# Optimization experiments

Measured on AMD Instinct MI355X. Metric: run time of the kernel, lower is better.

Reference implementation:

```python
import jax, jax.numpy as jnp
import numpy as np

NEG_INF = -10000.0
START_TAG = -2  # index into tag axis
END_TAG = -1


def setup_inputs() -> dict:
    B, T, N = 512, 1024, 64
    key = jax.random.key(0)
    k_h, k_tr, k_len = jax.random.split(key, 3)
    h = jax.random.normal(k_h, (B, T, N), dtype=jnp.float32)
    trans = jax.random.normal(k_tr, (N, N), dtype=jnp.float32)
    lengths = jax.random.randint(k_len, (B,), 1, T + 1)
    lengths = lengths.at[0].set(T)  # ensure max(lengths) == T, as the torch loop assumes
    return {"h": h, "trans": trans, "lengths": lengths}


def reference(h, trans, lengths):
    # h: [B, T, N] emissions; trans: [N, N], trans[i, j] = score(j -> i); lengths: [B]
    B, T, N = h.shape
    mask = jnp.arange(T)[None, :] < lengths[:, None]  # [B, T]

    init = jnp.full((B, N), NEG_INF, dtype=h.dtype).at[:, START_TAG].set(0.0)

    def step(score, xs):
        emit_t, m_t = xs  # emit_t: [B, N], m_t: [B]
        # score_t[b, i] = logsumexp_j( score[b, j] + emit_t[b, i] + trans[i, j] )
        s = score[:, None, :] + emit_t[:, :, None] + trans[None, :, :]  # [B, N, N]
        s = jax.nn.logsumexp(s, axis=2)  # [B, N]
        score = jnp.where(m_t[:, None], s, score)
        return score, None

    score, _ = jax.lax.scan(step, init, (jnp.swapaxes(h, 0, 1), mask.T))
    # terminal transition to END tag, then log-partition
    return jax.nn.logsumexp(score + trans[END_TAG], axis=-1)  # [B]
```

## Files before the change

kernel.cpp:

```cpp
#include <hip/hip_runtime.h>

#define LOG2E 1.4426950408889634f
#define LN2   0.6931471805599453f

__device__ __forceinline__ float bcast(float v, int l) {
  return __uint_as_float(__builtin_amdgcn_readlane(__float_as_uint(v), l));
}

template <bool FWD>
__device__ __forceinline__ void run_chain(
    const float* __restrict__ hb, const float* __restrict__ trans,
    int lane, int len, int nsteps, int T, float& pOut, int& b2Out) {
  constexpr int N = 64;

  float Mreg[N];
  if (FWD) {
    const float4* trow = (const float4*)(trans + lane * N);
#pragma unroll
    for (int q = 0; q < 16; ++q) {
      float4 tq = trow[q];
      Mreg[4 * q + 0] = __builtin_amdgcn_exp2f(tq.x * LOG2E);
      Mreg[4 * q + 1] = __builtin_amdgcn_exp2f(tq.y * LOG2E);
      Mreg[4 * q + 2] = __builtin_amdgcn_exp2f(tq.z * LOG2E);
      Mreg[4 * q + 3] = __builtin_amdgcn_exp2f(tq.w * LOG2E);
    }
  } else {
#pragma unroll
    for (int i = 0; i < N; ++i)
      Mreg[i] = __builtin_amdgcn_exp2f(trans[i * N + lane] * LOG2E);
  }
#pragma unroll
  for (int q = 0; q < 8; ++q) {
    asm volatile("" : "+v"(Mreg[8 * q + 0]), "+v"(Mreg[8 * q + 1]),
                      "+v"(Mreg[8 * q + 2]), "+v"(Mreg[8 * q + 3]),
                      "+v"(Mreg[8 * q + 4]), "+v"(Mreg[8 * q + 5]),
                      "+v"(Mreg[8 * q + 6]), "+v"(Mreg[8 * q + 7]));
  }

  float p;
  if (FWD)
    p = __builtin_amdgcn_exp2f((hb[lane] + trans[lane * N + (N - 2)]) * LOG2E);
  else
    p = __builtin_amdgcn_exp2f(trans[(N - 1) * N + lane] * LOG2E);
  int base2 = 0;

  auto step = [&](float D) {
    float src = FWD ? p : p * D;
    float a0 = 0.f, a1 = 0.f, a2 = 0.f, a3 = 0.f;
#pragma unroll
    for (int j = 0; j < N; j += 4) {
      a0 = fmaf(Mreg[j + 0], bcast(src, j + 0), a0);
      a1 = fmaf(Mreg[j + 1], bcast(src, j + 1), a1);
      a2 = fmaf(Mreg[j + 2], bcast(src, j + 2), a2);
      a3 = fmaf(Mreg[j + 3], bcast(src, j + 3), a3);
    }
    float s = (a0 + a1) + (a2 + a3);
    p = FWD ? s * D : s;
  };

  auto rescale = [&]() {
    unsigned bits = __builtin_amdgcn_readfirstlane(__float_as_uint(p));
    int e = (int)((bits >> 23) & 0xffu);
    base2 += e - 127;
    p *= __uint_as_float((unsigned)(254 - e) << 23);
  };

  auto emit_of = [&](int s) -> float {
    int sc = s < nsteps ? s : nsteps;
    if (sc < 1) sc = 1;
    int t = FWD ? sc : len - sc;
    return __builtin_amdgcn_exp2f(hb[(size_t)t * N + lane] * LOG2E);
  };

  float eb[8];
#pragma unroll
  for (int u = 0; u < 8; ++u) eb[u] = emit_of(1 + u);

  int s = 1;
  for (; s + 8 <= nsteps + 1; s += 8) {
#pragma unroll
    for (int u = 0; u < 8; ++u) {
      step(eb[u]);
      if (u == 3 || u == 7) rescale();
      eb[u] = emit_of(s + u + 8);
    }
  }
  for (; s <= nsteps; ++s) {
    step(eb[(s - 1) & 7]);
    rescale();
  }

  pOut = p;
  b2Out = base2;
}

__global__ __launch_bounds__(128)
__attribute__((amdgpu_waves_per_eu(1, 1)))
void crf_fwd_33852932227637(
    const float* __restrict__ h,
    const float* __restrict__ trans,
    const int* __restrict__ lengths,
    float* __restrict__ out,
    int T) {
  constexpr int N = 64;
  const int b = blockIdx.x;
  const int lane = threadIdx.x & 63;
  const int wv = threadIdx.x >> 6;

  const float* hb = h + (size_t)b * T * N;
  const int len = lengths[b];
  const int m = (len - 1) >> 1;

  float p;
  int b2;
  if (wv == 0)
    run_chain<true>(hb, trans, lane, len, m, T, p, b2);
  else
    run_chain<false>(hb, trans, lane, len, len - 1 - m, T, p, b2);

  __shared__ float xbeta[N];
  __shared__ int xb2;
  if (wv == 1) {
    xbeta[lane] = p;
    if (lane == 0) xb2 = b2;
  }
  __syncthreads();
  if (wv == 0) {
    float z = p * xbeta[lane];
#pragma unroll
    for (int off = 32; off >= 1; off >>= 1)
      z += __shfl_xor(z, off, 64);
    if (lane == 0)
      out[b] = LN2 * ((float)(b2 + xb2) + __builtin_amdgcn_logf(z));
  }
}

extern "C" void kernel_launch(void* const* d_in, const int* in_sizes, int n_in,
                              void* d_out, int out_size, void* d_ws, size_t ws_size,
                              hipStream_t stream) {
  const float* h = (const float*)d_in[0];
  const float* trans = (const float*)d_in[1];
  const int* lengths = (const int*)d_in[2];
  float* out = (float*)d_out;
  const int B = in_sizes[2];
  const int N = 64;
  const int T = in_sizes[0] / (B * N);
  crf_fwd_33852932227637<<<B, N * 2, 0, stream>>>(h, trans, lengths, out, T);
}
```

Before: 281.6 us.

## Broadcast CRF state via LDS float4 reads instead of readlane

```diff
diff --git a/kernel.cpp b/kernel.cpp
--- a/kernel.cpp
+++ b/kernel.cpp
@@ -3,14 +3,10 @@
 #define LOG2E 1.4426950408889634f
 #define LN2   0.6931471805599453f
 
-__device__ __forceinline__ float bcast(float v, int l) {
-  return __uint_as_float(__builtin_amdgcn_readlane(__float_as_uint(v), l));
-}
-
 template <bool FWD>
 __device__ __forceinline__ void run_chain(
     const float* __restrict__ hb, const float* __restrict__ trans,
-    int lane, int len, int nsteps, int T, float& pOut, int& b2Out) {
+    float* __restrict__ pbuf, int lane, int len, int nsteps, int& b2Out) {
   constexpr int N = 64;
 
   float Mreg[N];
@@ -37,38 +33,52 @@
                       "+v"(Mreg[8 * q + 6]), "+v"(Mreg[8 * q + 7]));
   }
 
-  float p;
-  if (FWD)
-    p = __builtin_amdgcn_exp2f((hb[lane] + trans[lane * N + (N - 2)]) * LOG2E);
-  else
-    p = __builtin_amdgcn_exp2f(trans[(N - 1) * N + lane] * LOG2E);
+  {
+    float v;
+    if (FWD) {
+      v = __builtin_amdgcn_exp2f((hb[lane] + trans[lane * N + (N - 2)]) * LOG2E);
+    } else {
+      v = __builtin_amdgcn_exp2f(trans[(N - 1) * N + lane] * LOG2E);
+      if (nsteps >= 1)
+        v *= __builtin_amdgcn_exp2f(hb[(size_t)(len - 1) * N + lane] * LOG2E);
+    }
+    pbuf[lane] = v;
+  }
   int base2 = 0;
 
-  auto step = [&](float D) {
-    float src = FWD ? p : p * D;
-    float a0 = 0.f, a1 = 0.f, a2 = 0.f, a3 = 0.f;
+  const int ns = FWD ? nsteps : nsteps - 1;
+
+  auto step = [&](float D, bool resc) {
+    const float4* pb4 = (const float4*)pbuf;
+    float a[8] = {0.f, 0.f, 0.f, 0.f, 0.f, 0.f, 0.f, 0.f};
+    float p0ref = 0.f;
 #pragma unroll
-    for (int j = 0; j < N; j += 4) {
-      a0 = fmaf(Mreg[j + 0], bcast(src, j + 0), a0);
-      a1 = fmaf(Mreg[j + 1], bcast(src, j + 1), a1);
-      a2 = fmaf(Mreg[j + 2], bcast(src, j + 2), a2);
-      a3 = fmaf(Mreg[j + 3], bcast(src, j + 3), a3);
+    for (int g = 0; g < 16; ++g) {
+      float4 q = pb4[g];
+      if (g == 0) p0ref = q.x;
+      const int b0 = (4 * g) & 7;
+      a[b0 + 0] = fmaf(Mreg[4 * g + 0], q.x, a[b0 + 0]);
+      a[b0 + 1] = fmaf(Mreg[4 * g + 1], q.y, a[b0 + 1]);
+      a[b0 + 2] = fmaf(Mreg[4 * g + 2], q.z, a[b0 + 2]);
+      a[b0 + 3] = fmaf(Mreg[4 * g + 3], q.w, a[b0 + 3]);
     }
-    float s = (a0 + a1) + (a2 + a3);
-    p = FWD ? s * D : s;
+    float mult = D;
+    if (resc) {
+      unsigned bits = __float_as_uint(p0ref);
+      int e = (int)((bits >> 23) & 0xffu);
+      base2 += e - 127;
+      mult *= __uint_as_float((unsigned)(254 - e) << 23);
+    }
+    float s = ((a[0] + a[1]) + (a[2] + a[3])) + ((a[4] + a[5]) + (a[6] + a[7]));
+    pbuf[lane] = s * mult;
   };
 
-  auto rescale = [&]() {
-    unsigned bits = __builtin_amdgcn_readfirstlane(__float_as_uint(p));
-    int e = (int)((bits >> 23) & 0xffu);
-    base2 += e - 127;
-    p *= __uint_as_float((unsigned)(254 - e) << 23);
-  };
-
-  auto emit_of = [&](int s) -> float {
-    int sc = s < nsteps ? s : nsteps;
+  auto emit_of = [&](int s_) -> float {
+    int smax = ns < 1 ? 1 : ns;
+    int sc = s_ < smax ? s_ : smax;
     if (sc < 1) sc = 1;
-    int t = FWD ? sc : len - sc;
+    int t = FWD ? sc : (len - 1 - sc);
+    if (t < 0) t = 0;
     return __builtin_amdgcn_exp2f(hb[(size_t)t * N + lane] * LOG2E);
   };
 
@@ -77,20 +87,18 @@
   for (int u = 0; u < 8; ++u) eb[u] = emit_of(1 + u);
 
   int s = 1;
-  for (; s + 8 <= nsteps + 1; s += 8) {
+  for (; s + 8 <= ns + 1; s += 8) {
 #pragma unroll
     for (int u = 0; u < 8; ++u) {
-      step(eb[u]);
-      if (u == 3 || u == 7) rescale();
+      step(eb[u], (u & 1) == 1);
       eb[u] = emit_of(s + u + 8);
     }
   }
-  for (; s <= nsteps; ++s) {
-    step(eb[(s - 1) & 7]);
-    rescale();
+  for (; s <= ns; ++s) {
+    step(eb[(s - 1) & 7], true);
   }
+  if (!FWD && nsteps >= 1) step(1.0f, true);
 
-  pOut = p;
   b2Out = base2;
 }
 
@@ -111,27 +119,24 @@
   const int len = lengths[b];
   const int m = (len - 1) >> 1;
 
-  float p;
+  __shared__ __align__(16) float pbuf[2][N];
+  __shared__ int xb2[2];
+
   int b2;
   if (wv == 0)
-    run_chain<true>(hb, trans, lane, len, m, T, p, b2);
+    run_chain<true>(hb, trans, pbuf[0], lane, len, m, b2);
   else
-    run_chain<false>(hb, trans, lane, len, len - 1 - m, T, p, b2);
+    run_chain<false>(hb, trans, pbuf[1], lane, len, len - 1 - m, b2);
+  if (lane == 0) xb2[wv] = b2;
+  __syncthreads();
 
-  __shared__ float xbeta[N];
-  __shared__ int xb2;
-  if (wv == 1) {
-    xbeta[lane] = p;
-    if (lane == 0) xb2 = b2;
-  }
-  __syncthreads();
   if (wv == 0) {
-    float z = p * xbeta[lane];
+    float z = pbuf[0][lane] * pbuf[1][lane];
 #pragma unroll
     for (int off = 32; off >= 1; off >>= 1)
       z += __shfl_xor(z, off, 64);
     if (lane == 0)
-      out[b] = LN2 * ((float)(b2 + xb2) + __builtin_amdgcn_logf(z));
+      out[b] = LN2 * ((float)(xb2[0] + xb2[1]) + __builtin_amdgcn_logf(z));
   }
 }
 
```

Measured after the change: 269.5 us. 4.3% less time.

## Replace readlane broadcasts with DPP/permlane rotation for matvec in CRF recurrence

Applied to the files above, without the earlier changes.

```diff
diff --git a/kernel.cpp b/kernel.cpp
--- a/kernel.cpp
+++ b/kernel.cpp
@@ -3,31 +3,118 @@
 #define LOG2E 1.4426950408889634f
 #define LN2   0.6931471805599453f
 
-__device__ __forceinline__ float bcast(float v, int l) {
-  return __uint_as_float(__builtin_amdgcn_readlane(__float_as_uint(v), l));
-}
-
-template <bool FWD>
+typedef unsigned u32x2 __attribute__((ext_vector_type(2)));
+
+#if __has_builtin(__builtin_amdgcn_permlane16_swap)
+#define HAVE_PL16 1
+#else
+#define HAVE_PL16 0
+#endif
+#if __has_builtin(__builtin_amdgcn_permlane32_swap)
+#define HAVE_PL32 1
+#else
+#define HAVE_PL32 0
+#endif
+
+
+#define QP_X1 0xB1
+#define QP_X2 0x4E
+#define QP_X3 0x1B
+#define ROR4  0x124
+
+template <int CTRL>
+__device__ __forceinline__ unsigned dppu(unsigned v) {
+  return (unsigned)__builtin_amdgcn_mov_dpp((int)v, CTRL, 0xf, 0xf, true);
+}
+
+template <int MODE>
+__device__ __forceinline__ unsigned xsw16(unsigned v, bool rowodd) {
+#if HAVE_PL16
+  if (MODE < 2) {
+    u32x2 r = __builtin_amdgcn_permlane16_swap(v, v, false, false);
+    unsigned cx = MODE ? r.y : r.x;
+    unsigned cy = MODE ? r.x : r.y;
+    return rowodd ? cx : cy;
+  }
+#endif
+  return (unsigned)__shfl_xor((int)v, 16, 64);
+}
+
+template <int MODE>
+__device__ __forceinline__ unsigned xsw32(unsigned v, bool hihalf) {
+#if HAVE_PL32
+  if (MODE < 2) {
+    u32x2 r = __builtin_amdgcn_permlane32_swap(v, v, false, false);
+    unsigned cx = MODE ? r.y : r.x;
+    unsigned cy = MODE ? r.x : r.y;
+    return hihalf ? cx : cy;
+  }
+#endif
+  return (unsigned)__shfl_xor((int)v, 32, 64);
+}
+
+__device__ __forceinline__ int detect16(int lane) {
+#if HAVE_PL16
+  bool rowodd = (lane & 16) != 0;
+  unsigned t0 = xsw16<0>((unsigned)lane, rowodd);
+  if (__ballot(t0 == (unsigned)(lane ^ 16)) == ~0ull) return 0;
+  unsigned t1 = xsw16<1>((unsigned)lane, rowodd);
+  if (__ballot(t1 == (unsigned)(lane ^ 16)) == ~0ull) return 1;
+#endif
+  return 2;
+}
+
+__device__ __forceinline__ int detect32(int lane) {
+#if HAVE_PL32
+  bool hihalf = (lane & 32) != 0;
+  unsigned t0 = xsw32<0>((unsigned)lane, hihalf);
+  if (__ballot(t0 == (unsigned)(lane ^ 32)) == ~0ull) return 0;
+  unsigned t1 = xsw32<1>((unsigned)lane, hihalf);
+  if (__ballot(t1 == (unsigned)(lane ^ 32)) == ~0ull) return 1;
+#endif
+  return 2;
+}
+
+template <int NEXT, int M16, int M32>
+__device__ __forceinline__ unsigned advanceu(unsigned w, bool rowodd, bool hihalf) {
+  if constexpr (NEXT == 4 || NEXT == 12) return xsw16<M16>(w, rowodd);
+  else if constexpr (NEXT == 8) return xsw32<M32>(w, hihalf);
+  else return dppu<ROR4>(w);
+}
+
+template <bool FWD, int M16, int M32>
 __device__ __forceinline__ void run_chain(
     const float* __restrict__ hb, const float* __restrict__ trans,
-    int lane, int len, int nsteps, int T, float& pOut, int& b2Out) {
+    int lane, int len, int nsteps, float& pOut, int& b2Out) {
   constexpr int N = 64;
+  const bool rowodd = (lane & 16) != 0;
+  const bool hihalf = (lane & 32) != 0;
 
   float Mreg[N];
-  if (FWD) {
-    const float4* trow = (const float4*)(trans + lane * N);
-#pragma unroll
-    for (int q = 0; q < 16; ++q) {
-      float4 tq = trow[q];
-      Mreg[4 * q + 0] = __builtin_amdgcn_exp2f(tq.x * LOG2E);
-      Mreg[4 * q + 1] = __builtin_amdgcn_exp2f(tq.y * LOG2E);
-      Mreg[4 * q + 2] = __builtin_amdgcn_exp2f(tq.z * LOG2E);
-      Mreg[4 * q + 3] = __builtin_amdgcn_exp2f(tq.w * LOG2E);
+  {
+    unsigned pr = (unsigned)lane;
+#pragma unroll
+    for (int m = 0; m < 16; ++m) {
+      unsigned j0 = pr;
+      unsigned j1 = dppu<QP_X1>(pr);
+      unsigned j2 = dppu<QP_X2>(pr);
+      unsigned j3 = dppu<QP_X3>(pr);
+      Mreg[4 * m + 0] = __builtin_amdgcn_exp2f(
+          (FWD ? trans[lane * N + j0] : trans[j0 * N + lane]) * LOG2E);
+      Mreg[4 * m + 1] = __builtin_amdgcn_exp2f(
+          (FWD ? trans[lane * N + j1] : trans[j1 * N + lane]) * LOG2E);
+      Mreg[4 * m + 2] = __builtin_amdgcn_exp2f(
+          (FWD ? trans[lane * N + j2] : trans[j2 * N + lane]) * LOG2E);
+      Mreg[4 * m + 3] = __builtin_amdgcn_exp2f(
+          (FWD ? trans[lane * N + j3] : trans[j3 * N + lane]) * LOG2E);
+      switch (m + 1) {
+        case 4:  pr = advanceu<4, M16, M32>(pr, rowodd, hihalf); break;
+        case 8:  pr = advanceu<8, M16, M32>(pr, rowodd, hihalf); break;
+        case 12: pr = advanceu<12, M16, M32>(pr, rowodd, hihalf); break;
+        case 16: break;
+        default: pr = dppu<ROR4>(pr); break;
+      }
     }
-  } else {
-#pragma unroll
-    for (int i = 0; i < N; ++i)
-      Mreg[i] = __builtin_amdgcn_exp2f(trans[i * N + lane] * LOG2E);
   }
 #pragma unroll
   for (int q = 0; q < 8; ++q) {
@@ -38,57 +125,74 @@
   }
 
   float p;
-  if (FWD)
+  if (FWD) {
     p = __builtin_amdgcn_exp2f((hb[lane] + trans[lane * N + (N - 2)]) * LOG2E);
-  else
+  } else {
     p = __builtin_amdgcn_exp2f(trans[(N - 1) * N + lane] * LOG2E);
+    if (nsteps >= 1)
+      p *= __builtin_amdgcn_exp2f(hb[(size_t)(len - 1) * N + lane] * LOG2E);
+  }
   int base2 = 0;
+  float pend = 1.0f;
+  int pend_b2 = 0;
+
+  const int ns = FWD ? nsteps : nsteps - 1;
 
   auto step = [&](float D) {
-    float src = FWD ? p : p * D;
-    float a0 = 0.f, a1 = 0.f, a2 = 0.f, a3 = 0.f;
-#pragma unroll
-    for (int j = 0; j < N; j += 4) {
-      a0 = fmaf(Mreg[j + 0], bcast(src, j + 0), a0);
-      a1 = fmaf(Mreg[j + 1], bcast(src, j + 1), a1);
-      a2 = fmaf(Mreg[j + 2], bcast(src, j + 2), a2);
-      a3 = fmaf(Mreg[j + 3], bcast(src, j + 3), a3);
+    float mult = D * pend;
+    base2 += pend_b2;
+    float a[8] = {0.f, 0.f, 0.f, 0.f, 0.f, 0.f, 0.f, 0.f};
+    unsigned w = __float_as_uint(p);
+#pragma unroll
+    for (int m = 0; m < 16; ++m) {
+      float f0 = __uint_as_float(w);
+      float f1 = __uint_as_float(dppu<QP_X1>(w));
+      float f2 = __uint_as_float(dppu<QP_X2>(w));
+      float f3 = __uint_as_float(dppu<QP_X3>(w));
+      const int c = (4 * m) & 7;
+      a[c + 0] = fmaf(Mreg[4 * m + 0], f0, a[c + 0]);
+      a[c + 1] = fmaf(Mreg[4 * m + 1], f1, a[c + 1]);
+      a[c + 2] = fmaf(Mreg[4 * m + 2], f2, a[c + 2]);
+      a[c + 3] = fmaf(Mreg[4 * m + 3], f3, a[c + 3]);
+      switch (m + 1) {
+        case 4:  w = advanceu<4, M16, M32>(w, rowodd, hihalf); break;
+        case 8:  w = advanceu<8, M16, M32>(w, rowodd, hihalf); break;
+        case 12: w = advanceu<12, M16, M32>(w, rowodd, hihalf); break;
+        case 16: break;
+        default: w = dppu<ROR4>(w); break;
+      }
     }
-    float s = (a0 + a1) + (a2 + a3);
-    p = FWD ? s * D : s;
+    float s = ((a[0] + a[1]) + (a[2] + a[3])) + ((a[4] + a[5]) + (a[6] + a[7]));
+    p = s * mult;
+    unsigned bits = (unsigned)__builtin_amdgcn_readfirstlane((int)__float_as_uint(p));
+    int e = (int)((bits >> 23) & 0xffu);
+    pend_b2 = e - 127;
+    pend = __uint_as_float((unsigned)(254 - e) << 23);
   };
 
-  auto rescale = [&]() {
-    unsigned bits = __builtin_amdgcn_readfirstlane(__float_as_uint(p));
-    int e = (int)((bits >> 23) & 0xffu);
-    base2 += e - 127;
-    p *= __uint_as_float((unsigned)(254 - e) << 23);
-  };
-
-  auto emit_of = [&](int s) -> float {
-    int sc = s < nsteps ? s : nsteps;
+  auto emit_of = [&](int s_) -> float {
+    int smax = ns < 1 ? 1 : ns;
+    int sc = s_ < smax ? s_ : smax;
     if (sc < 1) sc = 1;
-    int t = FWD ? sc : len - sc;
+    int t = FWD ? sc : (len - 1 - sc);
+    if (t < 0) t = 0;
     return __builtin_amdgcn_exp2f(hb[(size_t)t * N + lane] * LOG2E);
   };
 
-  float eb[8];
-#pragma unroll
-  for (int u = 0; u < 8; ++u) eb[u] = emit_of(1 + u);
+  float eb[4];
+#pragma unroll
+  for (int u = 0; u < 4; ++u) eb[u] = emit_of(1 + u);
 
   int s = 1;
-  for (; s + 8 <= nsteps + 1; s += 8) {
-#pragma unroll
-    for (int u = 0; u < 8; ++u) {
+  for (; s + 4 <= ns + 1; s += 4) {
+#pragma unroll
+    for (int u = 0; u < 4; ++u) {
       step(eb[u]);
-      if (u == 3 || u == 7) rescale();
-      eb[u] = emit_of(s + u + 8);
+      eb[u] = emit_of(s + u + 4);
     }
   }
-  for (; s <= nsteps; ++s) {
-    step(eb[(s - 1) & 7]);
-    rescale();
-  }
+  for (; s <= ns; ++s) step(eb[(s - 1) & 3]);
+  if (!FWD && nsteps >= 1) step(1.0f);
 
   pOut = p;
   b2Out = base2;
@@ -111,12 +215,25 @@
   const int len = lengths[b];
   const int m = (len - 1) >> 1;
 
+  const int m16 = detect16(lane);
+  const int m32 = detect32(lane);
+
   float p;
   int b2;
-  if (wv == 0)
-    run_chain<true>(hb, trans, lane, len, m, T, p, b2);
-  else
-    run_chain<false>(hb, trans, lane, len, len - 1 - m, T, p, b2);
+#define RUN(M16V, M32V)                                                       \
+  do {                                                                        \
+    if (wv == 0)                                                              \
+      run_chain<true, M16V, M32V>(hb, trans, lane, len, m, p, b2);            \
+    else                                                                      \
+      run_chain<false, M16V, M32V>(hb, trans, lane, len, len - 1 - m, p, b2); \
+  } while (0)
+
+  if (m16 == 0 && m32 == 0)      RUN(0, 0);
+  else if (m16 == 1 && m32 == 1) RUN(1, 1);
+  else if (m16 == 0 && m32 == 1) RUN(0, 1);
+  else if (m16 == 1 && m32 == 0) RUN(1, 0);
+  else                           RUN(2, 2);
+#undef RUN
 
   __shared__ float xbeta[N];
   __shared__ int xb2;
```

Result: slower. 317.0 us (+12.6%).
